# Kernel optimization log

Hardware: AMD Instinct MI355X
Metric: run time of the kernel (lower is better)

## Reference

```python
import jax, jax.numpy as jnp
import numpy as np

NUM_GROUPS = 16   # static upper bound on group ids (actual ids in [0, 12))
MIN_COUNT = 10    # min_subgroup_count


def setup_inputs() -> dict:
    key = jax.random.key(0)
    ks = jax.random.split(key, 7)
    B = 32768
    N = 16777216  # dataset_size
    probs = jax.random.uniform(ks[0], (B,), dtype=jnp.float32)
    labels = jax.random.randint(ks[1], (B,), 0, 2, dtype=jnp.int32)
    groups = jax.random.randint(ks[2], (B,), 0, 12, dtype=jnp.int32)
    indices = jax.random.randint(ks[3], (B,), 0, N, dtype=jnp.int32)
    # persistent buffers, pre-filled with valid mid-epoch state
    score_buffer = jax.random.uniform(ks[4], (N,), dtype=jnp.float32)
    label_buffer = jax.random.randint(ks[5], (N,), 0, 2, dtype=jnp.int32)
    group_buffer = jax.random.randint(ks[6], (N,), 0, 12, dtype=jnp.int32)
    return {"probs": probs, "labels": labels, "groups": groups, "indices": indices,
            "score_buffer": score_buffer, "label_buffer": label_buffer,
            "group_buffer": group_buffer}


def reference(probs, labels, groups, indices, score_buffer, label_buffer, group_buffer):
    # scatter current batch into dataset-sized buffers (functional clone + write)
    scores = score_buffer.at[indices].set(probs)
    labs = label_buffer.at[indices].set(labels)
    grps = group_buffer.at[indices].set(groups)

    valid = (~jnp.isnan(scores)) & (labs >= 0) & (grps >= 0)
    scores = jnp.where(valid, scores, 0.0)        # kill NaNs before weighted sums
    seg = jnp.where(valid, grps, 0)               # invalid rows get weight 0 anyway

    def group_var(lab_val):
        # per-group mean of scores restricted to (valid & label==lab_val),
        # then unbiased variance across groups meeting the min-count threshold
        w = (valid & (labs == lab_val)).astype(scores.dtype)
        sums = jax.ops.segment_sum(scores * w, seg, num_segments=NUM_GROUPS)
        cnts = jax.ops.segment_sum(w, seg, num_segments=NUM_GROUPS)
        avg = sums / jnp.maximum(cnts, 1.0)
        incl = (cnts >= MIN_COUNT).astype(scores.dtype)
        n = incl.sum()
        mean = (avg * incl).sum() / jnp.maximum(n, 1.0)
        var = (incl * (avg - mean) ** 2).sum() / jnp.maximum(n - 1.0, 1.0)  # ddof=1
        return var, n

    pos_var, n_pos = group_var(1)
    neg_var, n_neg = group_var(0)
    pos_ok = n_pos >= 2.0
    neg_ok = n_neg >= 2.0
    loss = jnp.where(pos_ok & neg_ok, 0.5 * (pos_var + neg_var),
                     jnp.where(pos_ok, pos_var,
                               jnp.where(neg_ok, neg_var, 0.0)))
    return loss
```

## Files before the change

### kernel.cpp

```cpp
#include <hip/hip_runtime.h>
#include <hip/hip_bf16.h>


#define TBL   65536u
#define TBLM  (TBL - 1u)
#define NGR   12
#define NBK   24
#define NCOL  25
#define CCOL  26
#define NTHR  256
#define CHUNK 16384
#define ITER  (CHUNK / 4 / NTHR)
#define UNR   4
#define MINC  10.0

__device__ __forceinline__ unsigned hash_idx(unsigned idx) {
    return (idx * 2654435761u) & TBLM;
}

__global__ void k_vote(const int* __restrict__ indices,
                       unsigned long long* __restrict__ table,
                       unsigned* __restrict__ bitmap, int B) {
    int b = blockIdx.x * blockDim.x + threadIdx.x;
    if (b >= B) return;
    unsigned idx = (unsigned)indices[b];
    atomicOr(&bitmap[idx >> 5], 1u << (idx & 31u));
    unsigned long long key = ((unsigned long long)(idx + 1u)) << 32;
    unsigned long long val = key | (unsigned long long)(unsigned)b;
    unsigned slot = hash_idx(idx);
    for (;;) {
        unsigned long long prev = atomicCAS(&table[slot], 0ULL, val);
        if (prev == 0ULL) return;
        if ((prev >> 32) == (unsigned long long)(idx + 1u)) {
            atomicMax(&table[slot], val);
            return;
        }
        slot = (slot + 1u) & TBLM;
    }
}

__global__ void k_resolve(const unsigned long long* __restrict__ table,
                          const float* __restrict__ probs,
                          const int* __restrict__ labels,
                          const int* __restrict__ groups,
                          float4* __restrict__ tbl2) {
    int s = blockIdx.x * blockDim.x + threadIdx.x;
    unsigned long long e = table[s];
    unsigned hi = (unsigned)(e >> 32);
    float4 r = make_float4(0.f, 0.f, 0.f, 0.f);
    if (hi) {
        int b = (int)(e & 0xffffffffu);
        r.x = probs[b];
        r.y = __int_as_float(labels[b]);
        r.z = __int_as_float(groups[b]);
        r.w = __uint_as_float(hi);
    }
    tbl2[s] = r;
}

__device__ __forceinline__ void apply_ovr(int idx, float& s, int& l, int& g,
        const float4* __restrict__ tbl2) {
    unsigned slot = hash_idx((unsigned)idx);
    unsigned hi = (unsigned)idx + 1u;
    for (;;) {
        float4 r = tbl2[slot];
        if (__float_as_uint(r.w) == hi) {
            s = r.x; l = __float_as_int(r.y); g = __float_as_int(r.z);
            return;
        }
        slot = (slot + 1u) & TBLM;
    }
}

__device__ __forceinline__ float ovr_s(int idx,
        const float4* __restrict__ tbl2) {
    unsigned slot = hash_idx((unsigned)idx);
    unsigned hi = (unsigned)idx + 1u;
    for (;;) {
        float4 r = tbl2[slot];
        if (__float_as_uint(r.w) == hi) return r.x;
        slot = (slot + 1u) & TBLM;
    }
}

__device__ __forceinline__ void quad_p1(float* __restrict__ row,
        unsigned* __restrict__ bstr32,
        float4 s4, int4 l4, int4 g4, unsigned bits, int v,
        const float4* __restrict__ tbl2) {
    float ss[4] = {s4.x, s4.y, s4.z, s4.w};
    int   ll[4] = {l4.x, l4.y, l4.z, l4.w};
    int   gg[4] = {g4.x, g4.y, g4.z, g4.w};
    if (bits & 0xFu) {
#pragma unroll
        for (int e = 0; e < 4; ++e)
            if ((bits >> e) & 1u)
                apply_ovr((v << 2) + e, ss[e], ll[e], gg[e], tbl2);
    }
    float val[4]; int bkt[4];
#pragma unroll
    for (int e = 0; e < 4; ++e) {
        bool valid = (ss[e] == ss[e]) && ((unsigned)ll[e] < 2u) &&
                     ((unsigned)gg[e] < (unsigned)NGR);
        bkt[e] = valid ? (gg[e] * 2 + ll[e]) : NBK;
        val[e] = valid ? ss[e] : 0.f;
    }
    bstr32[v] = (unsigned)bkt[0] | ((unsigned)bkt[1] << 8) |
                ((unsigned)bkt[2] << 16) | ((unsigned)bkt[3] << 24);
#define MRG(i, j) { bool m_ = (bkt[i] == bkt[j]); \
                    val[i] += m_ ? val[j] : 0.f;  \
                    bkt[j] = m_ ? NBK : bkt[j];   \
                    val[j] = m_ ? 0.f : val[j]; }
    MRG(0,1) MRG(0,2) MRG(0,3) MRG(1,2) MRG(1,3) MRG(2,3)
#undef MRG
    float a0 = row[bkt[0]], a1 = row[bkt[1]], a2 = row[bkt[2]], a3 = row[bkt[3]];
    row[bkt[0]] = a0 + val[0];
    row[bkt[1]] = a1 + val[1];
    row[bkt[2]] = a2 + val[2];
    row[bkt[3]] = a3 + val[3];
}

__global__ __launch_bounds__(NTHR, 4) void k_pass1(
        const float* __restrict__ sb, const int* __restrict__ lb,
        const int* __restrict__ gb, const unsigned* __restrict__ bitmap,
        const float4* __restrict__ tbl2,
        float* __restrict__ bsum, unsigned char* __restrict__ bstream,
        int n, int nblk) {
    __shared__ float s_acc[NTHR * NCOL];
    int tid = threadIdx.x, blk = blockIdx.x;
    for (int i = tid; i < NTHR * NCOL; i += NTHR) s_acc[i] = 0.f;
    __syncthreads();
    float* row = &s_acc[tid * NCOL];
    unsigned* bstr32 = (unsigned*)bstream;
    int vbase = (blk * CHUNK) >> 2, nv = n >> 2;
    if (vbase + (CHUNK >> 2) <= nv) {
        int v0 = vbase + tid;
        unsigned sh = (unsigned)((v0 & 7) * 4);
#pragma unroll
        for (int m = 0; m < ITER / UNR; ++m) {
            float4 s4[UNR]; int4 l4[UNR], g4[UNR]; unsigned bm[UNR];
#pragma unroll
            for (int u = 0; u < UNR; ++u) {
                int v = v0 + (m * UNR + u) * NTHR;
                s4[u] = ((const float4*)sb)[v];
                l4[u] = ((const int4*)lb)[v];
                g4[u] = ((const int4*)gb)[v];
                bm[u] = bitmap[v >> 3];
            }
            asm volatile("" ::: "memory");
#pragma unroll
            for (int u = 0; u < UNR; ++u) {
                int v = v0 + (m * UNR + u) * NTHR;
                quad_p1(row, bstr32, s4[u], l4[u], g4[u], bm[u] >> sh, v, tbl2);
            }
        }
    } else {
        for (int it = 0; it < ITER; ++it) {
            int v = vbase + it * NTHR + tid;
            if (v >= nv) break;
            float4 s4 = ((const float4*)sb)[v];
            int4   l4 = ((const int4*)lb)[v];
            int4   g4 = ((const int4*)gb)[v];
            unsigned bits = bitmap[v >> 3] >> ((v & 7) * 4);
            quad_p1(row, bstr32, s4, l4, g4, bits, v, tbl2);
        }
    }
    if (blk == nblk - 1) {
        for (int i = (nv << 2) + tid; i < n; i += NTHR) {
            float s = sb[i]; int l = lb[i], g = gb[i];
            if ((bitmap[i >> 5] >> (i & 31)) & 1u)
                apply_ovr(i, s, l, g, tbl2);
            bool valid = (s == s) && ((unsigned)l < 2u) && ((unsigned)g < (unsigned)NGR);
            int bk = valid ? (g * 2 + l) : NBK;
            bstream[i] = (unsigned char)bk;
            row[bk] += valid ? s : 0.f;
        }
    }
    __syncthreads();
    if (tid < NBK * 8) {
        int bkt = tid >> 3, sub = tid & 7;
        float sm = 0.f;
        for (int j = 0; j < 32; ++j) sm += s_acc[(sub * 32 + j) * NCOL + bkt];
        for (int d = 4; d >= 1; d >>= 1) sm += __shfl_down(sm, d, 8);
        if (!sub) bsum[bkt * nblk + blk] = sm;
    }
}

__global__ void k_scan(const float* __restrict__ bsum,
                       float* __restrict__ bpref, int nblk) {
    __shared__ double sc[NTHR];
    int t = threadIdx.x, k = blockIdx.x;
    const float* src = bsum  + (size_t)k * nblk;
    float*       dst = bpref + (size_t)k * nblk;
    double carry = 0.0;
    for (int s0 = 0; s0 < nblk; s0 += 4 * NTHR) {
        int i0 = s0 + 4 * t;
        float x0 = (i0 + 0 < nblk) ? src[i0 + 0] : 0.f;
        float x1 = (i0 + 1 < nblk) ? src[i0 + 1] : 0.f;
        float x2 = (i0 + 2 < nblk) ? src[i0 + 2] : 0.f;
        float x3 = (i0 + 3 < nblk) ? src[i0 + 3] : 0.f;
        double p0 = (double)x0, p1 = p0 + x1, p2 = p1 + x2, tot = p2 + x3;
        sc[t] = tot;
        __syncthreads();
        for (int st = 1; st < NTHR; st <<= 1) {
            double a = (t >= st) ? sc[t - st] : 0.0;
            __syncthreads();
            sc[t] += a;
            __syncthreads();
        }
        double excl = carry + sc[t] - tot;
        if (i0 + 0 < nblk) dst[i0 + 0] = (float)excl;
        if (i0 + 1 < nblk) dst[i0 + 1] = (float)(excl + p0);
        if (i0 + 2 < nblk) dst[i0 + 2] = (float)(excl + p1);
        if (i0 + 3 < nblk) dst[i0 + 3] = (float)(excl + p2);
        double bt = sc[NTHR - 1];
        __syncthreads();
        carry += bt;
    }
}

__device__ __forceinline__ double aload_d(const double* p) {
    unsigned long long u = __hip_atomic_load((const unsigned long long*)p,
                              __ATOMIC_RELAXED, __HIP_MEMORY_SCOPE_AGENT);
    return __longlong_as_double((long long)u);
}

__device__ __forceinline__ void quad_p2(float* __restrict__ row,
        unsigned short* __restrict__ crow,
        const float2* __restrict__ s_model,
        float4 s4, unsigned b4, unsigned obits, int v, int base,
        const float4* __restrict__ tbl2) {
    float ss[4] = {s4.x, s4.y, s4.z, s4.w};
    if (obits & 0xFu) {
#pragma unroll
        for (int e = 0; e < 4; ++e)
            if ((obits >> e) & 1u) ss[e] = ovr_s((v << 2) + e, tbl2);
    }
    float cv[4]; int bkt[4], cn[4];
#pragma unroll
    for (int e = 0; e < 4; ++e) {
        int idx = (v << 2) + e;
        int bk = (int)((b4 >> (8 * e)) & 0xFFu);
        float s = ss[e];
        float2 m = s_model[bk];
        float S = fmaf(m.y, (float)(idx - base), m.x);
        float T = S + s;
        unsigned ue = __float_as_uint(T) & 0x7f800000u;
        float c;
        if (ue < (24u << 23)) c = s;
        else {
            unsigned ub = ue - (23u << 23);
            float u    = __uint_as_float(ub);
            float uinv = __uint_as_float((254u << 23) - ub);
            c = u * rintf(s * uinv);
        }
        bool valid = bk < NBK;
        bkt[e] = bk;
        cv[e] = valid ? c : 0.f;
        cn[e] = valid ? 1 : 0;
    }
#define MRG(i, j) { bool m_ = (bkt[i] == bkt[j]); \
                    cv[i] += m_ ? cv[j] : 0.f;    \
                    cn[i] += m_ ? cn[j] : 0;      \
                    bkt[j] = m_ ? NBK : bkt[j];   \
                    cv[j] = m_ ? 0.f : cv[j];     \
                    cn[j] = m_ ? 0 : cn[j]; }
    MRG(0,1) MRG(0,2) MRG(0,3) MRG(1,2) MRG(1,3) MRG(2,3)
#undef MRG
    float a0 = row[bkt[0]], a1 = row[bkt[1]], a2 = row[bkt[2]], a3 = row[bkt[3]];
    row[bkt[0]] = a0 + cv[0];
    row[bkt[1]] = a1 + cv[1];
    row[bkt[2]] = a2 + cv[2];
    row[bkt[3]] = a3 + cv[3];
    unsigned short c0 = crow[bkt[0]], c1 = crow[bkt[1]],
                   c2 = crow[bkt[2]], c3 = crow[bkt[3]];
    crow[bkt[0]] = (unsigned short)(c0 + cn[0]);
    crow[bkt[1]] = (unsigned short)(c1 + cn[1]);
    crow[bkt[2]] = (unsigned short)(c2 + cn[2]);
    crow[bkt[3]] = (unsigned short)(c3 + cn[3]);
}

__global__ __launch_bounds__(NTHR, 4) void k_pass2(
        const float* __restrict__ sb,
        const unsigned char* __restrict__ bstream,
        const unsigned* __restrict__ bitmap,
        const float4* __restrict__ tbl2,
        const float* __restrict__ bsum, const float* __restrict__ bpref,
        double* __restrict__ acc_sum, double* __restrict__ acc_cnt,
        unsigned* __restrict__ done, float* __restrict__ out,
        int n, int nblk) {
    __shared__ float s_accv[NTHR * NCOL];
    __shared__ unsigned short s_cnt[NTHR * CCOL];
    __shared__ float2 s_model[NCOL];
    int tid = threadIdx.x, blk = blockIdx.x;
    for (int i = tid; i < NTHR * NCOL; i += NTHR) s_accv[i] = 0.f;
    for (int i = tid; i < NTHR * CCOL; i += NTHR) s_cnt[i] = 0;
    if (tid < NBK)
        s_model[tid] = make_float2(bpref[tid * nblk + blk],
                                   bsum[tid * nblk + blk] * (1.0f / CHUNK));
    if (tid == NBK) s_model[NBK] = make_float2(0.f, 0.f);
    __syncthreads();
    float* row = &s_accv[tid * NCOL];
    unsigned short* crow = &s_cnt[tid * CCOL];
    const unsigned* bstr32 = (const unsigned*)bstream;
    int base = blk * CHUNK;
    int vbase = base >> 2, nv = n >> 2;
    if (vbase + (CHUNK >> 2) <= nv) {
        int v0 = vbase + tid;
        unsigned sh = (unsigned)((v0 & 7) * 4);
#pragma unroll
        for (int m = 0; m < ITER / UNR; ++m) {
            float4 s4[UNR]; unsigned pk[UNR], bm[UNR];
#pragma unroll
            for (int u = 0; u < UNR; ++u) {
                int v = v0 + (m * UNR + u) * NTHR;
                s4[u] = ((const float4*)sb)[v];
                pk[u] = bstr32[v];
                bm[u] = bitmap[v >> 3];
            }
            asm volatile("" ::: "memory");
#pragma unroll
            for (int u = 0; u < UNR; ++u) {
                int v = v0 + (m * UNR + u) * NTHR;
                quad_p2(row, crow, s_model, s4[u], pk[u], bm[u] >> sh,
                        v, base, tbl2);
            }
        }
    } else {
        for (int it = 0; it < ITER; ++it) {
            int v = vbase + it * NTHR + tid;
            if (v >= nv) break;
            float4 s4 = ((const float4*)sb)[v];
            unsigned b4 = bstr32[v];
            unsigned bits = bitmap[v >> 3] >> ((v & 7) * 4);
            quad_p2(row, crow, s_model, s4, b4, bits, v, base, tbl2);
        }
    }
    if (blk == nblk - 1) {
        for (int i = (nv << 2) + tid; i < n; i += NTHR) {
            float s = sb[i];
            int bk = (int)bstream[i];
            if ((bitmap[i >> 5] >> (i & 31)) & 1u)
                s = ovr_s(i, tbl2);
            float2 m = s_model[bk];
            float S = fmaf(m.y, (float)(i - base), m.x);
            float T = S + s;
            unsigned ue = __float_as_uint(T) & 0x7f800000u;
            float c;
            if (ue < (24u << 23)) c = s;
            else {
                unsigned ub = ue - (23u << 23);
                float u    = __uint_as_float(ub);
                float uinv = __uint_as_float((254u << 23) - ub);
                c = u * rintf(s * uinv);
            }
            bool valid = bk < NBK;
            row[bk] += valid ? c : 0.f;
            crow[bk] = (unsigned short)(crow[bk] + (valid ? 1 : 0));
        }
    }
    __syncthreads();
    if (tid < NBK * 8) {
        int bkt = tid >> 3, sub = tid & 7;
        float sm = 0.f; unsigned cc = 0;
        for (int j = 0; j < 32; ++j) {
            int t2 = sub * 32 + j;
            sm += s_accv[t2 * NCOL + bkt];
            cc += s_cnt[t2 * CCOL + bkt];
        }
        for (int d = 4; d >= 1; d >>= 1) {
            sm += __shfl_down(sm, d, 8);
            cc += __shfl_down(cc, d, 8);
        }
        if (!sub) {
            atomicAdd(&acc_sum[bkt], (double)sm);
            atomicAdd(&acc_cnt[bkt], (double)cc);
        }
    }
    __syncthreads();
    if (tid == 0) {
        __threadfence();
        unsigned r = __hip_atomic_fetch_add(done, 1u, __ATOMIC_ACQ_REL,
                                            __HIP_MEMORY_SCOPE_AGENT);
        if (r == (unsigned)(gridDim.x - 1)) {
            double var[2], nn[2];
            for (int l = 0; l < 2; ++l) {
                double avg[NGR];
                double ncnt = 0.0, s = 0.0;
                for (int g = 0; g < NGR; ++g) {
                    double c  = aload_d(&acc_cnt[g * 2 + l]);
                    double sm = aload_d(&acc_sum[g * 2 + l]);
                    double a = sm / fmax(c, 1.0);
                    avg[g] = a;
                    if (c >= MINC) { ncnt += 1.0; s += a; }
                }
                double mean = s / fmax(ncnt, 1.0), v = 0.0;
                for (int g = 0; g < NGR; ++g) {
                    double c = aload_d(&acc_cnt[g * 2 + l]);
                    if (c >= MINC) { double d = avg[g] - mean; v += d * d; }
                }
                var[l] = v / fmax(ncnt - 1.0, 1.0);
                nn[l] = ncnt;
            }
            bool p = nn[1] >= 2.0, q = nn[0] >= 2.0;
            double loss = (p && q) ? 0.5 * (var[1] + var[0])
                        : (p ? var[1] : (q ? var[0] : 0.0));
            out[0] = (float)loss;
        }
    }
}

extern "C" void kernel_launch(void* const* d_in, const int* in_sizes, int n_in,
                              void* d_out, int out_size, void* d_ws, size_t ws_size,
                              hipStream_t stream) {
    const float* probs   = (const float*)d_in[0];
    const int*   labels  = (const int*)d_in[1];
    const int*   groups  = (const int*)d_in[2];
    const int*   indices = (const int*)d_in[3];
    const float* sb      = (const float*)d_in[4];
    const int*   lb      = (const int*)d_in[5];
    const int*   gb      = (const int*)d_in[6];
    int B = in_sizes[0];
    int n = in_sizes[4];
    int nblk   = (n + CHUNK - 1) / CHUNK;
    int nwords = (n + 31) / 32;

    char* ws = (char*)d_ws;
    size_t off = 0;
    unsigned long long* table = (unsigned long long*)(ws + off); off += (size_t)TBL * 8;
    unsigned* bitmap  = (unsigned*)(ws + off); off += (size_t)nwords * 4;
    off = (off + 15) & ~(size_t)15;
    double*   acc_sum = (double*)(ws + off);   off += NBK * 8;
    double*   acc_cnt = (double*)(ws + off);   off += NBK * 8;
    unsigned* done    = (unsigned*)(ws + off); off += 16;
    size_t zero_bytes = off;
    float4*   tbl2    = (float4*)(ws + off);   off += (size_t)TBL * 16;
    unsigned char* bstream = (unsigned char*)(ws + off);
    off += ((size_t)n + 15) & ~(size_t)15;
    float*    bsum    = (float*)(ws + off);    off += (size_t)nblk * NBK * 4;
    float*    bpref   = (float*)(ws + off);    off += (size_t)nblk * NBK * 4;

    hipMemsetAsync(d_ws, 0, zero_bytes, stream);

    dim3 bblk((B + NTHR - 1) / NTHR);
    hipLaunchKernelGGL(k_vote, bblk, dim3(NTHR), 0, stream,
                       indices, table, bitmap, B);
    hipLaunchKernelGGL(k_resolve, dim3(TBL / NTHR), dim3(NTHR), 0, stream,
                       table, probs, labels, groups, tbl2);
    hipLaunchKernelGGL(k_pass1, dim3(nblk), dim3(NTHR), 0, stream,
                       sb, lb, gb, bitmap, tbl2, bsum, bstream, n, nblk);
    hipLaunchKernelGGL(k_scan, dim3(NBK), dim3(NTHR), 0, stream,
                       bsum, bpref, nblk);
    hipLaunchKernelGGL(k_pass2, dim3(nblk), dim3(NTHR), 0, stream,
                       sb, bstream, bitmap, tbl2, bsum, bpref,
                       acc_sum, acc_cnt, done, (float*)d_out, n, nblk);
}
```

Baseline: 305.1 us.

## Software-pipeline streaming loads with inline asm and explicit vmcnt waits

Replaces the batched load-then-compute loops in both passes with a hand-unrolled rolling pipeline. Raw global_load instructions go through inline asm, and explicit s_waitcnt vmcnt counts keep 4 (pass1) or 6 (pass2) iterations of loads in flight while earlier ones are consumed. This is meant to hide memory latency continuously instead of stalling at each batch boundary. In exchange it raises register pressure, and the inline asm with manual wait counts is fragile: any extra vector-memory op inside quad_p1/quad_p2, such as the tbl2 override lookup or the bstream stores, would make the counts wrong.

After: 306.4 us. About the same (+0.4%).

```diff
diff --git a/kernel.cpp b/kernel.cpp
--- a/kernel.cpp
+++ b/kernel.cpp
@@ -11,12 +11,34 @@
 #define NTHR  256
 #define CHUNK 16384
 #define ITER  (CHUNK / 4 / NTHR)
-#define UNR   4
 #define MINC  10.0
+
+static_assert(ITER == 16, "pipeline is hand-unrolled for ITER==16");
 
 __device__ __forceinline__ unsigned hash_idx(unsigned idx) {
     return (idx * 2654435761u) & TBLM;
 }
+
+__device__ __forceinline__ float4 gldf4(const float4* p) {
+    float4 r;
+    asm volatile("global_load_dwordx4 %0, %1, off"
+                 : "=v"(r) : "v"(p) : "memory");
+    return r;
+}
+__device__ __forceinline__ int4 gldi4(const int4* p) {
+    int4 r;
+    asm volatile("global_load_dwordx4 %0, %1, off"
+                 : "=v"(r) : "v"(p) : "memory");
+    return r;
+}
+__device__ __forceinline__ unsigned gldu(const unsigned* p) {
+    unsigned r;
+    asm volatile("global_load_dword %0, %1, off"
+                 : "=v"(r) : "v"(p) : "memory");
+    return r;
+}
+#define VMW(N) do { asm volatile("s_waitcnt vmcnt(" #N ")" ::: "memory"); \
+                    __builtin_amdgcn_sched_barrier(0); } while (0)
 
 __global__ void k_vote(const int* __restrict__ indices,
                        unsigned long long* __restrict__ table,
@@ -135,24 +157,33 @@
     if (vbase + (CHUNK >> 2) <= nv) {
         int v0 = vbase + tid;
         unsigned sh = (unsigned)((v0 & 7) * 4);
-#pragma unroll
-        for (int m = 0; m < ITER / UNR; ++m) {
-            float4 s4[UNR]; int4 l4[UNR], g4[UNR]; unsigned bm[UNR];
-#pragma unroll
-            for (int u = 0; u < UNR; ++u) {
-                int v = v0 + (m * UNR + u) * NTHR;
-                s4[u] = ((const float4*)sb)[v];
-                l4[u] = ((const int4*)lb)[v];
-                g4[u] = ((const int4*)gb)[v];
-                bm[u] = bitmap[v >> 3];
-            }
-            asm volatile("" ::: "memory");
-#pragma unroll
-            for (int u = 0; u < UNR; ++u) {
-                int v = v0 + (m * UNR + u) * NTHR;
-                quad_p1(row, bstr32, s4[u], l4[u], g4[u], bm[u] >> sh, v, tbl2);
-            }
-        }
+        float4 S[4]; int4 L[4], G[4]; unsigned Bm[4];
+#define P1_ISSUE(it, sl) { int v_ = v0 + (it) * NTHR;              \
+        S[sl]  = gldf4((const float4*)sb + v_);                    \
+        L[sl]  = gldi4((const int4*)lb + v_);                      \
+        G[sl]  = gldi4((const int4*)gb + v_);                      \
+        Bm[sl] = gldu(bitmap + (v_ >> 3)); }
+#define P1_COMP(t, sl) quad_p1(row, bstr32, S[sl], L[sl], G[sl],   \
+                               Bm[sl] >> sh, v0 + (t) * NTHR, tbl2);
+        P1_ISSUE(0, 0) P1_ISSUE(1, 1) P1_ISSUE(2, 2)
+        P1_ISSUE(3, 3)  VMW(12); P1_COMP(0, 0)
+        P1_ISSUE(4, 0)  VMW(12); P1_COMP(1, 1)
+        P1_ISSUE(5, 1)  VMW(12); P1_COMP(2, 2)
+        P1_ISSUE(6, 2)  VMW(12); P1_COMP(3, 3)
+        P1_ISSUE(7, 3)  VMW(12); P1_COMP(4, 0)
+        P1_ISSUE(8, 0)  VMW(12); P1_COMP(5, 1)
+        P1_ISSUE(9, 1)  VMW(12); P1_COMP(6, 2)
+        P1_ISSUE(10, 2) VMW(12); P1_COMP(7, 3)
+        P1_ISSUE(11, 3) VMW(12); P1_COMP(8, 0)
+        P1_ISSUE(12, 0) VMW(12); P1_COMP(9, 1)
+        P1_ISSUE(13, 1) VMW(12); P1_COMP(10, 2)
+        P1_ISSUE(14, 2) VMW(12); P1_COMP(11, 3)
+        P1_ISSUE(15, 3) VMW(12); P1_COMP(12, 0)
+        VMW(8);  P1_COMP(13, 1)
+        VMW(4);  P1_COMP(14, 2)
+        VMW(0);  P1_COMP(15, 3)
+#undef P1_ISSUE
+#undef P1_COMP
     } else {
         for (int it = 0; it < ITER; ++it) {
             int v = vbase + it * NTHR + tid;
@@ -307,24 +338,33 @@
     if (vbase + (CHUNK >> 2) <= nv) {
         int v0 = vbase + tid;
         unsigned sh = (unsigned)((v0 & 7) * 4);
-#pragma unroll
-        for (int m = 0; m < ITER / UNR; ++m) {
-            float4 s4[UNR]; unsigned pk[UNR], bm[UNR];
-#pragma unroll
-            for (int u = 0; u < UNR; ++u) {
-                int v = v0 + (m * UNR + u) * NTHR;
-                s4[u] = ((const float4*)sb)[v];
-                pk[u] = bstr32[v];
-                bm[u] = bitmap[v >> 3];
-            }
-            asm volatile("" ::: "memory");
-#pragma unroll
-            for (int u = 0; u < UNR; ++u) {
-                int v = v0 + (m * UNR + u) * NTHR;
-                quad_p2(row, crow, s_model, s4[u], pk[u], bm[u] >> sh,
-                        v, base, tbl2);
-            }
-        }
+        float4 S[6]; unsigned K[6], Bm[6];
+#define P2_ISSUE(it, sl) { int v_ = v0 + (it) * NTHR;              \
+        S[sl]  = gldf4((const float4*)sb + v_);                    \
+        K[sl]  = gldu(bstr32 + v_);                                \
+        Bm[sl] = gldu(bitmap + (v_ >> 3)); }
+#define P2_COMP(t, sl) quad_p2(row, crow, s_model, S[sl], K[sl],   \
+                               Bm[sl] >> sh, v0 + (t) * NTHR, base, tbl2);
+        P2_ISSUE(0, 0) P2_ISSUE(1, 1) P2_ISSUE(2, 2)
+        P2_ISSUE(3, 3) P2_ISSUE(4, 4)
+        P2_ISSUE(5, 5)  VMW(15); P2_COMP(0, 0)
+        P2_ISSUE(6, 0)  VMW(15); P2_COMP(1, 1)
+        P2_ISSUE(7, 1)  VMW(15); P2_COMP(2, 2)
+        P2_ISSUE(8, 2)  VMW(15); P2_COMP(3, 3)
+        P2_ISSUE(9, 3)  VMW(15); P2_COMP(4, 4)
+        P2_ISSUE(10, 4) VMW(15); P2_COMP(5, 5)
+        P2_ISSUE(11, 5) VMW(15); P2_COMP(6, 0)
+        P2_ISSUE(12, 0) VMW(15); P2_COMP(7, 1)
+        P2_ISSUE(13, 1) VMW(15); P2_COMP(8, 2)
+        P2_ISSUE(14, 2) VMW(15); P2_COMP(9, 3)
+        P2_ISSUE(15, 3) VMW(15); P2_COMP(10, 4)
+        VMW(12); P2_COMP(11, 5)
+        VMW(9);  P2_COMP(12, 0)
+        VMW(6);  P2_COMP(13, 1)
+        VMW(3);  P2_COMP(14, 2)
+        VMW(0);  P2_COMP(15, 3)
+#undef P2_ISSUE
+#undef P2_COMP
     } else {
         for (int it = 0; it < ITER; ++it) {
             int v = vbase + it * NTHR + tid;
```

## Fuse all stages into one persistent kernel with grid barriers

Applied to the files above, without the earlier changes.

Replaces the five launches (vote, resolve, pass1, scan, pass2) with a single persistent kernel of 512 blocks that walks chunks in grid-stride loops and separates phases with atomic grid barriers. It also packs the override flag into bit 7 of each bstream byte, so pass 2 no longer reads the bitmap, and it splits the override table into 64-bit atomic loads. The goal is to remove launch gaps and tail effects between stages. In exchange it relies on all 512 blocks being co-resident for the spin barriers, and the fixed grid size may underuse or oversubscribe the device compared with one block per chunk.

Result: slower. 565.7 us (+85.4%).

```diff
diff --git a/kernel.cpp b/kernel.cpp
--- a/kernel.cpp
+++ b/kernel.cpp
@@ -9,6 +9,7 @@
 #define NCOL  25
 #define CCOL  26
 #define NTHR  256
+#define GSZ   512
 #define CHUNK 16384
 #define ITER  (CHUNK / 4 / NTHR)
 #define UNR   4
@@ -18,67 +19,73 @@
     return (idx * 2654435761u) & TBLM;
 }
 
-__global__ void k_vote(const int* __restrict__ indices,
-                       unsigned long long* __restrict__ table,
-                       unsigned* __restrict__ bitmap, int B) {
-    int b = blockIdx.x * blockDim.x + threadIdx.x;
-    if (b >= B) return;
-    unsigned idx = (unsigned)indices[b];
-    atomicOr(&bitmap[idx >> 5], 1u << (idx & 31u));
-    unsigned long long key = ((unsigned long long)(idx + 1u)) << 32;
-    unsigned long long val = key | (unsigned long long)(unsigned)b;
-    unsigned slot = hash_idx(idx);
+__device__ __forceinline__ unsigned aload_u32(const unsigned* p) {
+    return __hip_atomic_load(p, __ATOMIC_RELAXED, __HIP_MEMORY_SCOPE_AGENT);
+}
+__device__ __forceinline__ unsigned long long aload_u64(const unsigned long long* p) {
+    return __hip_atomic_load(p, __ATOMIC_RELAXED, __HIP_MEMORY_SCOPE_AGENT);
+}
+__device__ __forceinline__ void astore_u64(unsigned long long* p, unsigned long long v) {
+    __hip_atomic_store(p, v, __ATOMIC_RELAXED, __HIP_MEMORY_SCOPE_AGENT);
+}
+__device__ __forceinline__ float aload_f(const float* p) {
+    unsigned u = __hip_atomic_load((const unsigned*)p,
+                     __ATOMIC_RELAXED, __HIP_MEMORY_SCOPE_AGENT);
+    return __uint_as_float(u);
+}
+__device__ __forceinline__ void astore_f(float* p, float v) {
+    __hip_atomic_store((unsigned*)p, __float_as_uint(v),
+                       __ATOMIC_RELAXED, __HIP_MEMORY_SCOPE_AGENT);
+}
+__device__ __forceinline__ double aload_d(const double* p) {
+    unsigned long long u = __hip_atomic_load((const unsigned long long*)p,
+                              __ATOMIC_RELAXED, __HIP_MEMORY_SCOPE_AGENT);
+    return __longlong_as_double((long long)u);
+}
+
+__device__ __forceinline__ void gbar(unsigned* cnt, unsigned* flag, int nb) {
+    __syncthreads();
+    if (threadIdx.x == 0) {
+        unsigned r = __hip_atomic_fetch_add(cnt, 1u, __ATOMIC_ACQ_REL,
+                                            __HIP_MEMORY_SCOPE_AGENT);
+        if (r == (unsigned)(nb - 1)) {
+            __hip_atomic_store(flag, 1u, __ATOMIC_RELEASE,
+                               __HIP_MEMORY_SCOPE_AGENT);
+        } else {
+            while (!__hip_atomic_load(flag, __ATOMIC_ACQUIRE,
+                                      __HIP_MEMORY_SCOPE_AGENT))
+                __builtin_amdgcn_s_sleep(2);
+        }
+    }
+    __syncthreads();
+}
+
+__device__ __forceinline__ void apply_ovr2(int idx, float& s, int& l, int& g,
+        const unsigned long long* __restrict__ tbl2) {
+    unsigned slot = hash_idx((unsigned)idx);
+    unsigned want = (unsigned)idx + 1u;
     for (;;) {
-        unsigned long long prev = atomicCAS(&table[slot], 0ULL, val);
-        if (prev == 0ULL) return;
-        if ((prev >> 32) == (unsigned long long)(idx + 1u)) {
-            atomicMax(&table[slot], val);
+        unsigned long long hi2 = aload_u64(&tbl2[2 * slot + 1]);
+        if ((unsigned)(hi2 >> 32) == want) {
+            unsigned long long lo = aload_u64(&tbl2[2 * slot]);
+            s = __uint_as_float((unsigned)lo);
+            l = (int)(unsigned)(lo >> 32);
+            g = (int)(unsigned)hi2;
             return;
         }
         slot = (slot + 1u) & TBLM;
     }
 }
-
-__global__ void k_resolve(const unsigned long long* __restrict__ table,
-                          const float* __restrict__ probs,
-                          const int* __restrict__ labels,
-                          const int* __restrict__ groups,
-                          float4* __restrict__ tbl2) {
-    int s = blockIdx.x * blockDim.x + threadIdx.x;
-    unsigned long long e = table[s];
-    unsigned hi = (unsigned)(e >> 32);
-    float4 r = make_float4(0.f, 0.f, 0.f, 0.f);
-    if (hi) {
-        int b = (int)(e & 0xffffffffu);
-        r.x = probs[b];
-        r.y = __int_as_float(labels[b]);
-        r.z = __int_as_float(groups[b]);
-        r.w = __uint_as_float(hi);
-    }
-    tbl2[s] = r;
-}
-
-__device__ __forceinline__ void apply_ovr(int idx, float& s, int& l, int& g,
-        const float4* __restrict__ tbl2) {
+__device__ __forceinline__ float ovr_s2(int idx,
+        const unsigned long long* __restrict__ tbl2) {
     unsigned slot = hash_idx((unsigned)idx);
-    unsigned hi = (unsigned)idx + 1u;
+    unsigned want = (unsigned)idx + 1u;
     for (;;) {
-        float4 r = tbl2[slot];
-        if (__float_as_uint(r.w) == hi) {
-            s = r.x; l = __float_as_int(r.y); g = __float_as_int(r.z);
-            return;
-        }
-        slot = (slot + 1u) & TBLM;
-    }
-}
-
-__device__ __forceinline__ float ovr_s(int idx,
-        const float4* __restrict__ tbl2) {
-    unsigned slot = hash_idx((unsigned)idx);
-    unsigned hi = (unsigned)idx + 1u;
-    for (;;) {
-        float4 r = tbl2[slot];
-        if (__float_as_uint(r.w) == hi) return r.x;
+        unsigned long long hi2 = aload_u64(&tbl2[2 * slot + 1]);
+        if ((unsigned)(hi2 >> 32) == want) {
+            unsigned long long lo = aload_u64(&tbl2[2 * slot]);
+            return __uint_as_float((unsigned)lo);
+        }
         slot = (slot + 1u) & TBLM;
     }
 }
@@ -86,7 +93,7 @@
 __device__ __forceinline__ void quad_p1(float* __restrict__ row,
         unsigned* __restrict__ bstr32,
         float4 s4, int4 l4, int4 g4, unsigned bits, int v,
-        const float4* __restrict__ tbl2) {
+        const unsigned long long* __restrict__ tbl2) {
     float ss[4] = {s4.x, s4.y, s4.z, s4.w};
     int   ll[4] = {l4.x, l4.y, l4.z, l4.w};
     int   gg[4] = {g4.x, g4.y, g4.z, g4.w};
@@ -94,7 +101,7 @@
 #pragma unroll
         for (int e = 0; e < 4; ++e)
             if ((bits >> e) & 1u)
-                apply_ovr((v << 2) + e, ss[e], ll[e], gg[e], tbl2);
+                apply_ovr2((v << 2) + e, ss[e], ll[e], gg[e], tbl2);
     }
     float val[4]; int bkt[4];
 #pragma unroll
@@ -104,8 +111,10 @@
         bkt[e] = valid ? (gg[e] * 2 + ll[e]) : NBK;
         val[e] = valid ? ss[e] : 0.f;
     }
-    bstr32[v] = (unsigned)bkt[0] | ((unsigned)bkt[1] << 8) |
-                ((unsigned)bkt[2] << 16) | ((unsigned)bkt[3] << 24);
+    bstr32[v] = ((unsigned)bkt[0] | (((bits >> 0) & 1u) << 7))
+              | (((unsigned)bkt[1] | (((bits >> 1) & 1u) << 7)) << 8)
+              | (((unsigned)bkt[2] | (((bits >> 2) & 1u) << 7)) << 16)
+              | (((unsigned)bkt[3] | (((bits >> 3) & 1u) << 7)) << 24);
 #define MRG(i, j) { bool m_ = (bkt[i] == bkt[j]); \
                     val[i] += m_ ? val[j] : 0.f;  \
                     bkt[j] = m_ ? NBK : bkt[j];   \
@@ -119,127 +128,22 @@
     row[bkt[3]] = a3 + val[3];
 }
 
-__global__ __launch_bounds__(NTHR, 4) void k_pass1(
-        const float* __restrict__ sb, const int* __restrict__ lb,
-        const int* __restrict__ gb, const unsigned* __restrict__ bitmap,
-        const float4* __restrict__ tbl2,
-        float* __restrict__ bsum, unsigned char* __restrict__ bstream,
-        int n, int nblk) {
-    __shared__ float s_acc[NTHR * NCOL];
-    int tid = threadIdx.x, blk = blockIdx.x;
-    for (int i = tid; i < NTHR * NCOL; i += NTHR) s_acc[i] = 0.f;
-    __syncthreads();
-    float* row = &s_acc[tid * NCOL];
-    unsigned* bstr32 = (unsigned*)bstream;
-    int vbase = (blk * CHUNK) >> 2, nv = n >> 2;
-    if (vbase + (CHUNK >> 2) <= nv) {
-        int v0 = vbase + tid;
-        unsigned sh = (unsigned)((v0 & 7) * 4);
-#pragma unroll
-        for (int m = 0; m < ITER / UNR; ++m) {
-            float4 s4[UNR]; int4 l4[UNR], g4[UNR]; unsigned bm[UNR];
-#pragma unroll
-            for (int u = 0; u < UNR; ++u) {
-                int v = v0 + (m * UNR + u) * NTHR;
-                s4[u] = ((const float4*)sb)[v];
-                l4[u] = ((const int4*)lb)[v];
-                g4[u] = ((const int4*)gb)[v];
-                bm[u] = bitmap[v >> 3];
-            }
-            asm volatile("" ::: "memory");
-#pragma unroll
-            for (int u = 0; u < UNR; ++u) {
-                int v = v0 + (m * UNR + u) * NTHR;
-                quad_p1(row, bstr32, s4[u], l4[u], g4[u], bm[u] >> sh, v, tbl2);
-            }
-        }
-    } else {
-        for (int it = 0; it < ITER; ++it) {
-            int v = vbase + it * NTHR + tid;
-            if (v >= nv) break;
-            float4 s4 = ((const float4*)sb)[v];
-            int4   l4 = ((const int4*)lb)[v];
-            int4   g4 = ((const int4*)gb)[v];
-            unsigned bits = bitmap[v >> 3] >> ((v & 7) * 4);
-            quad_p1(row, bstr32, s4, l4, g4, bits, v, tbl2);
-        }
-    }
-    if (blk == nblk - 1) {
-        for (int i = (nv << 2) + tid; i < n; i += NTHR) {
-            float s = sb[i]; int l = lb[i], g = gb[i];
-            if ((bitmap[i >> 5] >> (i & 31)) & 1u)
-                apply_ovr(i, s, l, g, tbl2);
-            bool valid = (s == s) && ((unsigned)l < 2u) && ((unsigned)g < (unsigned)NGR);
-            int bk = valid ? (g * 2 + l) : NBK;
-            bstream[i] = (unsigned char)bk;
-            row[bk] += valid ? s : 0.f;
-        }
-    }
-    __syncthreads();
-    if (tid < NBK * 8) {
-        int bkt = tid >> 3, sub = tid & 7;
-        float sm = 0.f;
-        for (int j = 0; j < 32; ++j) sm += s_acc[(sub * 32 + j) * NCOL + bkt];
-        for (int d = 4; d >= 1; d >>= 1) sm += __shfl_down(sm, d, 8);
-        if (!sub) bsum[bkt * nblk + blk] = sm;
-    }
-}
-
-__global__ void k_scan(const float* __restrict__ bsum,
-                       float* __restrict__ bpref, int nblk) {
-    __shared__ double sc[NTHR];
-    int t = threadIdx.x, k = blockIdx.x;
-    const float* src = bsum  + (size_t)k * nblk;
-    float*       dst = bpref + (size_t)k * nblk;
-    double carry = 0.0;
-    for (int s0 = 0; s0 < nblk; s0 += 4 * NTHR) {
-        int i0 = s0 + 4 * t;
-        float x0 = (i0 + 0 < nblk) ? src[i0 + 0] : 0.f;
-        float x1 = (i0 + 1 < nblk) ? src[i0 + 1] : 0.f;
-        float x2 = (i0 + 2 < nblk) ? src[i0 + 2] : 0.f;
-        float x3 = (i0 + 3 < nblk) ? src[i0 + 3] : 0.f;
-        double p0 = (double)x0, p1 = p0 + x1, p2 = p1 + x2, tot = p2 + x3;
-        sc[t] = tot;
-        __syncthreads();
-        for (int st = 1; st < NTHR; st <<= 1) {
-            double a = (t >= st) ? sc[t - st] : 0.0;
-            __syncthreads();
-            sc[t] += a;
-            __syncthreads();
-        }
-        double excl = carry + sc[t] - tot;
-        if (i0 + 0 < nblk) dst[i0 + 0] = (float)excl;
-        if (i0 + 1 < nblk) dst[i0 + 1] = (float)(excl + p0);
-        if (i0 + 2 < nblk) dst[i0 + 2] = (float)(excl + p1);
-        if (i0 + 3 < nblk) dst[i0 + 3] = (float)(excl + p2);
-        double bt = sc[NTHR - 1];
-        __syncthreads();
-        carry += bt;
-    }
-}
-
-__device__ __forceinline__ double aload_d(const double* p) {
-    unsigned long long u = __hip_atomic_load((const unsigned long long*)p,
-                              __ATOMIC_RELAXED, __HIP_MEMORY_SCOPE_AGENT);
-    return __longlong_as_double((long long)u);
-}
-
 __device__ __forceinline__ void quad_p2(float* __restrict__ row,
         unsigned short* __restrict__ crow,
         const float2* __restrict__ s_model,
-        float4 s4, unsigned b4, unsigned obits, int v, int base,
-        const float4* __restrict__ tbl2) {
+        float4 s4, unsigned b4, int v, int base,
+        const unsigned long long* __restrict__ tbl2) {
     float ss[4] = {s4.x, s4.y, s4.z, s4.w};
-    if (obits & 0xFu) {
+    if (b4 & 0x80808080u) {
 #pragma unroll
         for (int e = 0; e < 4; ++e)
-            if ((obits >> e) & 1u) ss[e] = ovr_s((v << 2) + e, tbl2);
+            if ((b4 >> (8 * e + 7)) & 1u) ss[e] = ovr_s2((v << 2) + e, tbl2);
     }
     float cv[4]; int bkt[4], cn[4];
 #pragma unroll
     for (int e = 0; e < 4; ++e) {
         int idx = (v << 2) + e;
-        int bk = (int)((b4 >> (8 * e)) & 0xFFu);
+        int bk = (int)((b4 >> (8 * e)) & 0x7Fu);
         float s = ss[e];
         float2 m = s_model[bk];
         float S = fmaf(m.y, (float)(idx - base), m.x);
@@ -279,124 +183,262 @@
     crow[bkt[3]] = (unsigned short)(c3 + cn[3]);
 }
 
-__global__ __launch_bounds__(NTHR, 4) void k_pass2(
-        const float* __restrict__ sb,
-        const unsigned char* __restrict__ bstream,
-        const unsigned* __restrict__ bitmap,
-        const float4* __restrict__ tbl2,
-        const float* __restrict__ bsum, const float* __restrict__ bpref,
+__global__ __launch_bounds__(NTHR, 4) void k_mega(
+        const float* __restrict__ sb, const int* __restrict__ lb,
+        const int* __restrict__ gb,
+        const float* __restrict__ probs, const int* __restrict__ labels,
+        const int* __restrict__ groups, const int* __restrict__ indices,
+        unsigned long long* __restrict__ table, unsigned* __restrict__ bitmap,
+        unsigned long long* __restrict__ tbl2,
+        float* __restrict__ bsum, float* __restrict__ bpref,
+        unsigned char* __restrict__ bstream,
         double* __restrict__ acc_sum, double* __restrict__ acc_cnt,
-        unsigned* __restrict__ done, float* __restrict__ out,
-        int n, int nblk) {
-    __shared__ float s_accv[NTHR * NCOL];
+        unsigned* __restrict__ bars, unsigned* __restrict__ done,
+        float* __restrict__ out, int B, int n, int nchk) {
+    __shared__ __align__(16) float s_acc[NTHR * NCOL];
     __shared__ unsigned short s_cnt[NTHR * CCOL];
     __shared__ float2 s_model[NCOL];
     int tid = threadIdx.x, blk = blockIdx.x;
-    for (int i = tid; i < NTHR * NCOL; i += NTHR) s_accv[i] = 0.f;
-    for (int i = tid; i < NTHR * CCOL; i += NTHR) s_cnt[i] = 0;
-    if (tid < NBK)
-        s_model[tid] = make_float2(bpref[tid * nblk + blk],
-                                   bsum[tid * nblk + blk] * (1.0f / CHUNK));
-    if (tid == NBK) s_model[NBK] = make_float2(0.f, 0.f);
-    __syncthreads();
-    float* row = &s_accv[tid * NCOL];
-    unsigned short* crow = &s_cnt[tid * CCOL];
-    const unsigned* bstr32 = (const unsigned*)bstream;
-    int base = blk * CHUNK;
-    int vbase = base >> 2, nv = n >> 2;
-    if (vbase + (CHUNK >> 2) <= nv) {
-        int v0 = vbase + tid;
-        unsigned sh = (unsigned)((v0 & 7) * 4);
-#pragma unroll
-        for (int m = 0; m < ITER / UNR; ++m) {
-            float4 s4[UNR]; unsigned pk[UNR], bm[UNR];
-#pragma unroll
-            for (int u = 0; u < UNR; ++u) {
-                int v = v0 + (m * UNR + u) * NTHR;
-                s4[u] = ((const float4*)sb)[v];
-                pk[u] = bstr32[v];
-                bm[u] = bitmap[v >> 3];
-            }
-            asm volatile("" ::: "memory");
-#pragma unroll
-            for (int u = 0; u < UNR; ++u) {
-                int v = v0 + (m * UNR + u) * NTHR;
-                quad_p2(row, crow, s_model, s4[u], pk[u], bm[u] >> sh,
-                        v, base, tbl2);
-            }
-        }
-    } else {
-        for (int it = 0; it < ITER; ++it) {
-            int v = vbase + it * NTHR + tid;
-            if (v >= nv) break;
-            float4 s4 = ((const float4*)sb)[v];
-            unsigned b4 = bstr32[v];
-            unsigned bits = bitmap[v >> 3] >> ((v & 7) * 4);
-            quad_p2(row, crow, s_model, s4, b4, bits, v, base, tbl2);
-        }
-    }
-    if (blk == nblk - 1) {
-        for (int i = (nv << 2) + tid; i < n; i += NTHR) {
-            float s = sb[i];
-            int bk = (int)bstream[i];
-            if ((bitmap[i >> 5] >> (i & 31)) & 1u)
-                s = ovr_s(i, tbl2);
-            float2 m = s_model[bk];
-            float S = fmaf(m.y, (float)(i - base), m.x);
-            float T = S + s;
-            unsigned ue = __float_as_uint(T) & 0x7f800000u;
-            float c;
-            if (ue < (24u << 23)) c = s;
-            else {
-                unsigned ub = ue - (23u << 23);
-                float u    = __uint_as_float(ub);
-                float uinv = __uint_as_float((254u << 23) - ub);
-                c = u * rintf(s * uinv);
-            }
-            bool valid = bk < NBK;
-            row[bk] += valid ? c : 0.f;
-            crow[bk] = (unsigned short)(crow[bk] + (valid ? 1 : 0));
-        }
-    }
-    __syncthreads();
-    if (tid < NBK * 8) {
-        int bkt = tid >> 3, sub = tid & 7;
-        float sm = 0.f; unsigned cc = 0;
-        for (int j = 0; j < 32; ++j) {
-            int t2 = sub * 32 + j;
-            sm += s_accv[t2 * NCOL + bkt];
-            cc += s_cnt[t2 * CCOL + bkt];
-        }
-        for (int d = 4; d >= 1; d >>= 1) {
-            sm += __shfl_down(sm, d, 8);
-            cc += __shfl_down(cc, d, 8);
-        }
-        if (!sub) {
-            atomicAdd(&acc_sum[bkt], (double)sm);
-            atomicAdd(&acc_cnt[bkt], (double)cc);
-        }
-    }
-    __syncthreads();
+    int gsz = (int)gridDim.x;
+    unsigned* bstr32 = (unsigned*)bstream;
+    int nv = n >> 2;
+
+    for (int b = blk * NTHR + tid; b < B; b += gsz * NTHR) {
+        unsigned idx = (unsigned)indices[b];
+        atomicOr(&bitmap[idx >> 5], 1u << (idx & 31u));
+        unsigned long long key = ((unsigned long long)(idx + 1u)) << 32;
+        unsigned long long val = key | (unsigned long long)(unsigned)b;
+        unsigned slot = hash_idx(idx);
+        for (;;) {
+            unsigned long long prev = atomicCAS(&table[slot], 0ULL, val);
+            if (prev == 0ULL) break;
+            if ((prev >> 32) == (unsigned long long)(idx + 1u)) {
+                atomicMax(&table[slot], val);
+                break;
+            }
+            slot = (slot + 1u) & TBLM;
+        }
+    }
+    gbar(&bars[0], &bars[1], gsz);
+
+    for (int s = blk * NTHR + tid; s < (int)TBL; s += gsz * NTHR) {
+        unsigned long long e = aload_u64(&table[s]);
+        unsigned hi = (unsigned)(e >> 32);
+        unsigned long long lo = 0ULL, h2 = 0ULL;
+        if (hi) {
+            int b = (int)(e & 0xffffffffu);
+            lo = (unsigned long long)__float_as_uint(probs[b])
+               | ((unsigned long long)(unsigned)labels[b] << 32);
+            h2 = (unsigned long long)(unsigned)groups[b]
+               | ((unsigned long long)hi << 32);
+        }
+        astore_u64(&tbl2[2 * s + 0], lo);
+        astore_u64(&tbl2[2 * s + 1], h2);
+    }
+    gbar(&bars[2], &bars[3], gsz);
+
+    for (int c = blk; c < nchk; c += gsz) {
+        for (int i = tid; i < NTHR * NCOL; i += NTHR) s_acc[i] = 0.f;
+        __syncthreads();
+        float* row = &s_acc[tid * NCOL];
+        int vbase = (c * CHUNK) >> 2;
+        if (vbase + (CHUNK >> 2) <= nv) {
+            int v0 = vbase + tid;
+            unsigned sh = (unsigned)((v0 & 7) * 4);
+#pragma unroll
+            for (int m = 0; m < ITER / UNR; ++m) {
+                float4 s4[UNR]; int4 l4[UNR], g4[UNR]; unsigned bm[UNR];
+#pragma unroll
+                for (int u = 0; u < UNR; ++u) {
+                    int v = v0 + (m * UNR + u) * NTHR;
+                    s4[u] = ((const float4*)sb)[v];
+                    l4[u] = ((const int4*)lb)[v];
+                    g4[u] = ((const int4*)gb)[v];
+                    bm[u] = aload_u32(bitmap + (v >> 3));
+                }
+                asm volatile("" ::: "memory");
+#pragma unroll
+                for (int u = 0; u < UNR; ++u) {
+                    int v = v0 + (m * UNR + u) * NTHR;
+                    quad_p1(row, bstr32, s4[u], l4[u], g4[u],
+                            bm[u] >> sh, v, tbl2);
+                }
+            }
+        } else {
+            for (int it = 0; it < ITER; ++it) {
+                int v = vbase + it * NTHR + tid;
+                if (v >= nv) break;
+                float4 s4 = ((const float4*)sb)[v];
+                int4   l4 = ((const int4*)lb)[v];
+                int4   g4 = ((const int4*)gb)[v];
+                unsigned bits = aload_u32(bitmap + (v >> 3)) >> ((v & 7) * 4);
+                quad_p1(row, bstr32, s4, l4, g4, bits, v, tbl2);
+            }
+        }
+        if (c == nchk - 1) {
+            for (int i = (nv << 2) + tid; i < n; i += NTHR) {
+                float s = sb[i]; int l = lb[i], g = gb[i];
+                unsigned ob = (aload_u32(bitmap + (i >> 5)) >> (i & 31)) & 1u;
+                if (ob) apply_ovr2(i, s, l, g, tbl2);
+                bool valid = (s == s) && ((unsigned)l < 2u) &&
+                             ((unsigned)g < (unsigned)NGR);
+                int bk = valid ? (g * 2 + l) : NBK;
+                bstream[i] = (unsigned char)(bk | (ob << 7));
+                row[bk] += valid ? s : 0.f;
+            }
+        }
+        __syncthreads();
+        if (tid < NBK * 8) {
+            int bkt = tid >> 3, sub = tid & 7;
+            float sm = 0.f;
+            for (int j = 0; j < 32; ++j)
+                sm += s_acc[(sub * 32 + j) * NCOL + bkt];
+            for (int d = 4; d >= 1; d >>= 1) sm += __shfl_down(sm, d, 8);
+            if (!sub) astore_f(&bsum[bkt * nchk + c], sm);
+        }
+        __syncthreads();
+    }
+    gbar(&bars[4], &bars[5], gsz);
+
+    if (blk < NBK) {
+        double* sc = (double*)s_acc;
+        const float* src = bsum  + (size_t)blk * nchk;
+        float*       dst = bpref + (size_t)blk * nchk;
+        double carry = 0.0;
+        for (int s0 = 0; s0 < nchk; s0 += 4 * NTHR) {
+            int i0 = s0 + 4 * tid;
+            float x0 = (i0 + 0 < nchk) ? aload_f(src + i0 + 0) : 0.f;
+            float x1 = (i0 + 1 < nchk) ? aload_f(src + i0 + 1) : 0.f;
+            float x2 = (i0 + 2 < nchk) ? aload_f(src + i0 + 2) : 0.f;
+            float x3 = (i0 + 3 < nchk) ? aload_f(src + i0 + 3) : 0.f;
+            double p0 = (double)x0, p1 = p0 + x1, p2 = p1 + x2, tot = p2 + x3;
+            sc[tid] = tot;
+            __syncthreads();
+            for (int st = 1; st < NTHR; st <<= 1) {
+                double a = (tid >= st) ? sc[tid - st] : 0.0;
+                __syncthreads();
+                sc[tid] += a;
+                __syncthreads();
+            }
+            double excl = carry + sc[tid] - tot;
+            if (i0 + 0 < nchk) astore_f(dst + i0 + 0, (float)excl);
+            if (i0 + 1 < nchk) astore_f(dst + i0 + 1, (float)(excl + p0));
+            if (i0 + 2 < nchk) astore_f(dst + i0 + 2, (float)(excl + p1));
+            if (i0 + 3 < nchk) astore_f(dst + i0 + 3, (float)(excl + p2));
+            double bt = sc[NTHR - 1];
+            __syncthreads();
+            carry += bt;
+        }
+    }
+    gbar(&bars[6], &bars[7], gsz);
+
+    for (int c = blk; c < nchk; c += gsz) {
+        for (int i = tid; i < NTHR * NCOL; i += NTHR) s_acc[i] = 0.f;
+        {
+            unsigned* cz = (unsigned*)s_cnt;
+            for (int i = tid; i < NTHR * CCOL / 2; i += NTHR) cz[i] = 0u;
+        }
+        if (tid < NBK)
+            s_model[tid] = make_float2(aload_f(&bpref[tid * nchk + c]),
+                                       aload_f(&bsum[tid * nchk + c])
+                                           * (1.0f / CHUNK));
+        if (tid == NBK) s_model[NBK] = make_float2(0.f, 0.f);
+        __syncthreads();
+        float* row = &s_acc[tid * NCOL];
+        unsigned short* crow = &s_cnt[tid * CCOL];
+        int base = c * CHUNK;
+        int vbase = base >> 2;
+        if (vbase + (CHUNK >> 2) <= nv) {
+            int v0 = vbase + tid;
+#pragma unroll
+            for (int m = 0; m < ITER / UNR; ++m) {
+                float4 s4[UNR]; unsigned pk[UNR];
+#pragma unroll
+                for (int u = 0; u < UNR; ++u) {
+                    int v = v0 + (m * UNR + u) * NTHR;
+                    s4[u] = ((const float4*)sb)[v];
+                    pk[u] = bstr32[v];
+                }
+                asm volatile("" ::: "memory");
+#pragma unroll
+                for (int u = 0; u < UNR; ++u) {
+                    int v = v0 + (m * UNR + u) * NTHR;
+                    quad_p2(row, crow, s_model, s4[u], pk[u], v, base, tbl2);
+                }
+            }
+        } else {
+            for (int it = 0; it < ITER; ++it) {
+                int v = vbase + it * NTHR + tid;
+                if (v >= nv) break;
+                float4 s4 = ((const float4*)sb)[v];
+                unsigned b4 = bstr32[v];
+                quad_p2(row, crow, s_model, s4, b4, v, base, tbl2);
+            }
+        }
+        if (c == nchk - 1) {
+            for (int i = (nv << 2) + tid; i < n; i += NTHR) {
+                float s = sb[i];
+                unsigned byte = bstream[i];
+                int bk = (int)(byte & 0x7Fu);
+                if (byte & 0x80u) s = ovr_s2(i, tbl2);
+                float2 m = s_model[bk];
+                float S = fmaf(m.y, (float)(i - base), m.x);
+                float T = S + s;
+                unsigned ue = __float_as_uint(T) & 0x7f800000u;
+                float cc;
+                if (ue < (24u << 23)) cc = s;
+                else {
+                    unsigned ub = ue - (23u << 23);
+                    float u    = __uint_as_float(ub);
+                    float uinv = __uint_as_float((254u << 23) - ub);
+                    cc = u * rintf(s * uinv);
+                }
+                bool valid = bk < NBK;
+                row[bk] += valid ? cc : 0.f;
+                crow[bk] = (unsigned short)(crow[bk] + (valid ? 1 : 0));
+            }
+        }
+        __syncthreads();
+        if (tid < NBK * 8) {
+            int bkt = tid >> 3, sub = tid & 7;
+            float sm = 0.f; unsigned cc = 0;
+            for (int j = 0; j < 32; ++j) {
+                int t2 = sub * 32 + j;
+                sm += s_acc[t2 * NCOL + bkt];
+                cc += s_cnt[t2 * CCOL + bkt];
+            }
+            for (int d = 4; d >= 1; d >>= 1) {
+                sm += __shfl_down(sm, d, 8);
+                cc += __shfl_down(cc, d, 8);
+            }
+            if (!sub) {
+                atomicAdd(&acc_sum[bkt], (double)sm);
+                atomicAdd(&acc_cnt[bkt], (double)cc);
+            }
+        }
+        __syncthreads();
+    }
+
     if (tid == 0) {
         __threadfence();
         unsigned r = __hip_atomic_fetch_add(done, 1u, __ATOMIC_ACQ_REL,
                                             __HIP_MEMORY_SCOPE_AGENT);
-        if (r == (unsigned)(gridDim.x - 1)) {
+        if (r == (unsigned)(gsz - 1)) {
             double var[2], nn[2];
             for (int l = 0; l < 2; ++l) {
                 double avg[NGR];
                 double ncnt = 0.0, s = 0.0;
                 for (int g = 0; g < NGR; ++g) {
-                    double c  = aload_d(&acc_cnt[g * 2 + l]);
+                    double cc = aload_d(&acc_cnt[g * 2 + l]);
                     double sm = aload_d(&acc_sum[g * 2 + l]);
-                    double a = sm / fmax(c, 1.0);
+                    double a = sm / fmax(cc, 1.0);
                     avg[g] = a;
-                    if (c >= MINC) { ncnt += 1.0; s += a; }
+                    if (cc >= MINC) { ncnt += 1.0; s += a; }
                 }
                 double mean = s / fmax(ncnt, 1.0), v = 0.0;
                 for (int g = 0; g < NGR; ++g) {
-                    double c = aload_d(&acc_cnt[g * 2 + l]);
-                    if (c >= MINC) { double d = avg[g] - mean; v += d * d; }
+                    double cc = aload_d(&acc_cnt[g * 2 + l]);
+                    if (cc >= MINC) { double d = avg[g] - mean; v += d * d; }
                 }
                 var[l] = v / fmax(ncnt - 1.0, 1.0);
                 nn[l] = ncnt;
@@ -421,7 +463,7 @@
     const int*   gb      = (const int*)d_in[6];
     int B = in_sizes[0];
     int n = in_sizes[4];
-    int nblk   = (n + CHUNK - 1) / CHUNK;
+    int nchk   = (n + CHUNK - 1) / CHUNK;
     int nwords = (n + 31) / 32;
 
     char* ws = (char*)d_ws;
@@ -432,25 +474,20 @@
     double*   acc_sum = (double*)(ws + off);   off += NBK * 8;
     double*   acc_cnt = (double*)(ws + off);   off += NBK * 8;
     unsigned* done    = (unsigned*)(ws + off); off += 16;
+    unsigned* bars    = (unsigned*)(ws + off); off += 8 * 4;
     size_t zero_bytes = off;
-    float4*   tbl2    = (float4*)(ws + off);   off += (size_t)TBL * 16;
+    unsigned long long* tbl2 = (unsigned long long*)(ws + off);
+    off += (size_t)TBL * 16;
     unsigned char* bstream = (unsigned char*)(ws + off);
     off += ((size_t)n + 15) & ~(size_t)15;
-    float*    bsum    = (float*)(ws + off);    off += (size_t)nblk * NBK * 4;
-    float*    bpref   = (float*)(ws + off);    off += (size_t)nblk * NBK * 4;
+    float*    bsum    = (float*)(ws + off);    off += (size_t)nchk * NBK * 4;
+    float*    bpref   = (float*)(ws + off);    off += (size_t)nchk * NBK * 4;
 
     hipMemsetAsync(d_ws, 0, zero_bytes, stream);
 
-    dim3 bblk((B + NTHR - 1) / NTHR);
-    hipLaunchKernelGGL(k_vote, bblk, dim3(NTHR), 0, stream,
-                       indices, table, bitmap, B);
-    hipLaunchKernelGGL(k_resolve, dim3(TBL / NTHR), dim3(NTHR), 0, stream,
-                       table, probs, labels, groups, tbl2);
-    hipLaunchKernelGGL(k_pass1, dim3(nblk), dim3(NTHR), 0, stream,
-                       sb, lb, gb, bitmap, tbl2, bsum, bstream, n, nblk);
-    hipLaunchKernelGGL(k_scan, dim3(NBK), dim3(NTHR), 0, stream,
-                       bsum, bpref, nblk);
-    hipLaunchKernelGGL(k_pass2, dim3(nblk), dim3(NTHR), 0, stream,
-                       sb, bstream, bitmap, tbl2, bsum, bpref,
-                       acc_sum, acc_cnt, done, (float*)d_out, n, nblk);
-}
+    hipLaunchKernelGGL(k_mega, dim3(GSZ), dim3(NTHR), 0, stream,
+                       sb, lb, gb, probs, labels, groups, indices,
+                       table, bitmap, tbl2, bsum, bpref, bstream,
+                       acc_sum, acc_cnt, bars, done, (float*)d_out,
+                       B, n, nchk);
+}
```
